# Performance work log

Measured on AMD Instinct MI355X. Metric: run time of the kernel, lower is better.

## Reference

```python
import jax, jax.numpy as jnp
import numpy as np

N = 50000      # amino-acid nodes
DIN = 64       # input feature dim
DH = 64        # hidden dim (= GAT out_feats per head)
H = 4          # attention heads
E_RES, E_SEQ, E_KNN = 400000, 100000, 400000
EPS = 1e-5


def setup_inputs() -> dict:
    key = jax.random.key(0)
    ks = iter(jax.random.split(key, 32))
    def nrm(shape, scale=0.1):
        return jax.random.normal(next(ks), shape, dtype=jnp.float32) * scale
    def edges(E):
        s = jax.random.randint(next(ks), (E,), 0, N, dtype=jnp.int32)
        d = jax.random.randint(next(ks), (E,), 0, N, dtype=jnp.int32)
        return s, d
    x = nrm((N, DIN), 1.0)
    src_res, dst_res = edges(E_RES)
    src_seq, dst_seq = edges(E_SEQ)
    src_knn, dst_knn = edges(E_KNN)
    inp = dict(x=x, src_res=src_res, dst_res=dst_res, src_seq=src_seq,
               dst_seq=dst_seq, src_knn=src_knn, dst_knn=dst_knn)
    # layer 0 (in=DIN), layer 1 (in=DH): per-relation stacked GAT params
    inp.update(W0=nrm((3, DIN, H * DH)), al0=nrm((3, H, DH)), ar0=nrm((3, H, DH)),
               b0=nrm((3, H * DH)), rW0=nrm((3, DIN, H * DH)))
    inp.update(W1=nrm((3, DH, H * DH)), al1=nrm((3, H, DH)), ar1=nrm((3, H, DH)),
               b1=nrm((3, H * DH)), rW1=nrm((3, DH, H * DH)))
    inp.update(fcW0=nrm((DH, DH)), fcb0=nrm((DH,)), fcW1=nrm((DH, DH)), fcb1=nrm((DH,)))
    inp.update(g0=jnp.ones((DIN,), jnp.float32), be0=jnp.zeros((DIN,), jnp.float32),
               g1=jnp.ones((DH,), jnp.float32), be1=jnp.zeros((DH,), jnp.float32))
    return inp


def _bn(x, g, b):
    mu = jnp.mean(x, axis=0)
    var = jnp.mean((x - mu) ** 2, axis=0)
    return (x - mu) * jax.lax.rsqrt(var + EPS) * g + b


def _gat(h, src, dst, W, al, ar, bias, rW):
    # DGL GATConv (feat_drop off in eval, residual=True via res_fc Linear, bias)
    n = h.shape[0]
    fs = (h @ W).reshape(n, H, DH)                    # [N,H,D]
    el = jnp.sum(fs * al, axis=-1)                    # [N,H]
    er = jnp.sum(fs * ar, axis=-1)
    e = jax.nn.leaky_relu(el[src] + er[dst], 0.2)     # [E,H]
    m = jax.ops.segment_max(e, dst, num_segments=n)
    a = jnp.exp(e - m[dst])
    s = jax.ops.segment_sum(a, dst, num_segments=n)
    alpha = a / s[dst]                                # edge-softmax per dst/head
    rst = jax.ops.segment_sum(alpha[:, :, None] * fs[src], dst, num_segments=n)
    return rst + (h @ rW).reshape(n, H, DH) + bias.reshape(1, H, DH)


def _layer(x, edges, W, al, ar, b, rW, fcW, fcb, g, be):
    x = _bn(x, g, be)
    h = jnp.zeros((x.shape[0], H, DH), x.dtype)
    for r, (s_, d_) in enumerate(edges):              # 3 relation types, summed
        h = h + _gat(x, s_, d_, W[r], al[r], ar[r], b[r], rW[r])
    x = jnp.mean(h, axis=1)                           # mean over heads
    return jax.nn.relu(x @ fcW + fcb)


def reference(x, src_res, dst_res, src_seq, dst_seq, src_knn, dst_knn,
              W0, al0, ar0, b0, rW0, W1, al1, ar1, b1, rW1,
              fcW0, fcb0, fcW1, fcb1, g0, be0, g1, be1):
    edges = [(src_res, dst_res), (src_seq, dst_seq), (src_knn, dst_knn)]
    x = _layer(x, edges, W0, al0, ar0, b0, rW0, fcW0, fcb0, g0, be0)
    x = _layer(x, edges, W1, al1, ar1, b1, rW1, fcW1, fcb1, g1, be1)
    return x
```

## Files before the change

### kernel.cpp

```cpp
#include <hip/hip_runtime.h>
#include <math.h>

#define NN    50000
#define DD    64
#define HH    4
#define E_RES 400000
#define E_SEQ 100000
#define E_KNN 400000
#define ETOT  (E_RES+E_SEQ+E_KNN)
#define RPS   (NN + 4)
#define NBLK  ((NN+255)/256)
#define KTOT  864
#define CTPS  (ETOT + 32)
#define NBUK  98
#define TBUK  (3*NBUK)
#define EPB   4096
#define PABLK ((ETOT+EPB-1)/EPB)
#define FBLK  (NN/16)
#define LZS   810

typedef __attribute__((ext_vector_type(8))) short short8;
typedef __attribute__((ext_vector_type(4))) float floatx4;

__device__ inline unsigned short f2bf(float f){
  union{float f; unsigned u;} v; v.f=f;
  unsigned r = v.u + 0x7FFF + ((v.u>>16)&1);
  return (unsigned short)(r>>16);
}
__device__ inline float bf2f(unsigned short u){
  union{unsigned u; float f;} v; v.u=(unsigned)u<<16; return v.f;
}

__global__ void __launch_bounds__(256)
k_bucketcnt(const int* __restrict__ d0, const int* __restrict__ d1,
            const int* __restrict__ d2, int* __restrict__ bcnt){
  __shared__ int cnt[TBUK];
  int t = threadIdx.x;
  for(int i=t;i<TBUK;i+=256) cnt[i]=0;
  __syncthreads();
  int ebase = blockIdx.x*EPB;
  #pragma unroll
  for(int j=0;j<16;j++){
    int i = ebase + j*256 + t;
    int d, r;
    if(i < E_RES){ d=d0[i]; r=0; }
    else if(i < E_RES+E_SEQ){ d=d1[i-E_RES]; r=1; }
    else if(i < ETOT){ d=d2[i-E_RES-E_SEQ]; r=2; }
    else continue;
    atomicAdd(&cnt[r*NBUK + (d>>9)], 1);
  }
  __syncthreads();
  for(int i=t;i<TBUK;i+=256){ int c=cnt[i]; if(c) atomicAdd(&bcnt[i], c); }
}

__global__ void k_bucketscan(const int* __restrict__ bcnt,
                             int* __restrict__ bbase, int* __restrict__ bcur){
  __shared__ int sh[TBUK];
  int t = threadIdx.x;
  if(t < 64){
    int carry = 0;
    for(int c=0;c<5;c++){
      int idx = c*64 + t;
      int v = (idx < TBUK) ? bcnt[idx] : 0;
      int inc = v;
      for(int off=1; off<64; off<<=1){ int n=__shfl_up(inc, off, 64); if(t>=off) inc+=n; }
      if(idx < TBUK) sh[idx] = carry + inc - v;
      carry += __shfl(inc, 63, 64);
    }
  }
  __syncthreads();
  if(t < TBUK){ bbase[t] = sh[t]; bcur[t] = sh[t]; }
  if(t == 0) bbase[TBUK] = ETOT;
}

__global__ void __launch_bounds__(256)
k_partA(const int* __restrict__ s0, const int* __restrict__ d0,
        const int* __restrict__ s1, const int* __restrict__ d1,
        const int* __restrict__ s2, const int* __restrict__ d2,
        int* __restrict__ bcur, unsigned* __restrict__ pairs){
  __shared__ int cnt[TBUK];
  __shared__ int gb[TBUK];
  int t = threadIdx.x;
  for(int i=t;i<TBUK;i+=256) cnt[i]=0;
  __syncthreads();
  int ebase = blockIdx.x*EPB;
  unsigned meta[16], pk[16];
  #pragma unroll
  for(int j=0;j<16;j++){
    int i = ebase + j*256 + t;
    int s, d, r;
    if(i < E_RES){ s=s0[i]; d=d0[i]; r=0; }
    else if(i < E_RES+E_SEQ){ int k=i-E_RES; s=s1[k]; d=d1[k]; r=1; }
    else if(i < ETOT){ int k=i-E_RES-E_SEQ; s=s2[k]; d=d2[k]; r=2; }
    else { meta[j]=0xFFFFFFFFu; continue; }
    int bk = r*NBUK + (d>>9);
    int rk = atomicAdd(&cnt[bk], 1);
    meta[j] = ((unsigned)bk<<16) | (unsigned)rk;
    pk[j]   = ((unsigned)(d&511)<<16) | (unsigned)s;
  }
  __syncthreads();
  for(int i=t;i<TBUK;i+=256){ int c=cnt[i]; gb[i] = c ? atomicAdd(&bcur[i], c) : 0; }
  __syncthreads();
  #pragma unroll
  for(int j=0;j<16;j++){
    unsigned mt = meta[j];
    if(mt != 0xFFFFFFFFu)
      pairs[gb[mt>>16] + (mt & 0xFFFFu)] = pk[j];
  }
}

__global__ void __launch_bounds__(256)
k_partB(const unsigned* __restrict__ pairs, const int* __restrict__ bbase,
        int* __restrict__ rowptr, int* __restrict__ csr){
  int bb = blockIdx.x, r = bb / NBUK, b = bb - r*NBUK;
  int dbase = b*512, dmax = min(512, NN - dbase);
  int off = (r==0)?0:(r==1)?E_RES:(E_RES+E_SEQ);
  __shared__ int hist[512];
  __shared__ int curs[513];
  int t = threadIdx.x;
  hist[t]=0; hist[256+t]=0;
  __syncthreads();
  int beg = bbase[bb], end = bbase[bb+1];
  for(int i=beg+t; i<end; i+=256) atomicAdd(&hist[pairs[i]>>16], 1);
  __syncthreads();
  if(t < 64){
    int carry = 0;
    for(int c=0;c<8;c++){
      int v = hist[c*64+t];
      int inc = v;
      for(int o2=1; o2<64; o2<<=1){ int n=__shfl_up(inc, o2, 64); if(t>=o2) inc+=n; }
      curs[c*64+t] = (beg - off) + carry + inc - v;
      carry += __shfl(inc, 63, 64);
    }
    if(t==0) curs[512] = end - off;
  }
  __syncthreads();
  int* rp = rowptr + r*RPS + dbase;
  for(int i=t; i<=dmax; i+=256) rp[i] = curs[i];
  __syncthreads();
  for(int i=beg+t; i<end; i+=256){
    unsigned p = pairs[i];
    int pos = atomicAdd(&curs[p>>16], 1);
    csr[off + pos] = (int)(p & 0xFFFFu);
  }
}

__global__ void k_bnstats(const float* __restrict__ x, float* __restrict__ stats,
                          unsigned short* __restrict__ Abf){
  __shared__ float sh[512];
  int t = threadIdx.x, col = t & 63, rg = t >> 6;
  float s=0.f, q=0.f;
  for(int row = blockIdx.x*4 + rg; row < NN; row += gridDim.x*4){
    float v = x[(size_t)row*64 + col]; s += v; q += v*v;
    Abf[(size_t)row*64 + col] = f2bf(v);
  }
  sh[t]=s; sh[256+t]=q; __syncthreads();
  if(rg==0){
    s = sh[col]+sh[64+col]+sh[128+col]+sh[192+col];
    q = sh[256+col]+sh[320+col]+sh[384+col]+sh[448+col];
    atomicAdd(&stats[col], s); atomicAdd(&stats[64+col], q);
  }
}

__global__ void __launch_bounds__(256)
k_prep3(const float* __restrict__ stats, const float* __restrict__ g,
        const float* __restrict__ be, const float* __restrict__ W,
        const float* __restrict__ al, const float* __restrict__ ar,
        const float* __restrict__ b, const float* __restrict__ rW,
        const float* __restrict__ fcW, const float* __restrict__ fcb,
        float* __restrict__ wbufF){
  __shared__ float scale[64], shift[64];
  int t = threadIdx.x;
  if(t<64){
    float mu  = stats[t]*(1.0f/NN);
    float var = stats[64+t]*(1.0f/NN) - mu*mu;
    float sc  = g[t]*rsqrtf(var + 1e-5f);
    scale[t]=sc; shift[t]=be[t]-mu*sc;
  }
  __syncthreads();
  char* wb = (char*)wbufF;
  unsigned short* Wf = (unsigned short*)wbufF;
  float* biasF = (float*)(wb + 110592);
  int bid = blockIdx.x;
  if(bid < 52){
    __shared__ float fcWs[4096];
    for(int i=t;i<4096;i+=256) fcWs[i]=fcW[i];
    __syncthreads();
    int j = bid*16 + (t>>4);
    int cg = (t&15)*4;
    float Wrow[64];
    if(j < 64){
      for(int d=0; d<64; d++){
        float w=0.f;
        for(int r=0;r<3;r++)
          #pragma unroll
          for(int h=0;h<4;h++)
            w += rW[((size_t)(r*64+j))*256 + h*64 + d];
        Wrow[d] = scale[j]*0.25f*w;
      }
    } else {
      int jj = j-64;
      int r = jj>>8, dc = jj&255, h = dc&3, c = dc>>2;
      const float* Wp = W + ((size_t)(r*64+c))*256 + h*64;
      float sc = 0.25f*scale[c];
      #pragma unroll
      for(int d=0; d<64; d++) Wrow[d] = sc*Wp[d];
    }
    #pragma unroll
    for(int cc=0; cc<4; cc++){
      int col = cg+cc;
      float acc=0.f;
      #pragma unroll
      for(int d=0; d<64; d++) acc += Wrow[d]*fcWs[d*64+col];
      Wf[(size_t)col*KTOT + j] = f2bf(acc);
    }
  } else if(bid < 58){
    int wv = (bid-52)*4 + (t>>6);
    int r = wv >> 3, cc = wv & 7, h = cc & 3, k = t & 63;
    const float* av = ((cc>=4)?ar:al) + (r*HH+h)*64;
    const float* Wk = W + ((size_t)(r*64+k))*256 + h*64;
    float w=0.f;
    for(int d2=0; d2<64; d2++) w += Wk[d2]*av[d2];
    float* WelR = (float*)(wb + 110848 + r*2080);
    WelR[cc*64 + k] = scale[k]*w;
    float bp = shift[k]*w;
    for(int off=32; off; off>>=1) bp += __shfl_down(bp, off, 64);
    if(k==0) (WelR + 512)[cc] = bp;
  } else {
    __shared__ float S[3][64];
    __shared__ float BH[64];
    if(t<192){
      int r=t>>6, d=t&63;
      float s=0.f;
      #pragma unroll
      for(int h=0;h<4;h++){
        const float* Wp = W + (size_t)(r*64)*256 + h*64 + d;
        for(int k=0;k<64;k++) s += shift[k]*Wp[(size_t)k*256];
      }
      S[r][d]=0.25f*s;
    } else {
      int d = t-192;
      float s=0.f;
      for(int k=0;k<64;k++){
        float w=0.f;
        for(int r=0;r<3;r++)
          #pragma unroll
          for(int h=0;h<4;h++)
            w += rW[((size_t)(r*64+k))*256 + h*64 + d];
        s += shift[k]*0.25f*w;
      }
      float bb=0.f;
      for(int r=0;r<3;r++)
        #pragma unroll
        for(int h=0;h<4;h++) bb += b[r*256 + h*64 + d];
      BH[d] = s + 0.25f*bb;
    }
    __syncthreads();
    if(t<192){
      int r=t>>6, col=t&63;
      float acc=0.f;
      for(int d=0;d<64;d++) acc += S[r][d]*fcW[d*64+col];
      Wf[(size_t)col*KTOT + 832 + r] = f2bf(acc);
    } else {
      int col=t-192;
      float acc=0.f;
      for(int d=0;d<64;d++) acc += BH[d]*fcW[d*64+col];
      biasF[col] = acc + fcb[col];
    }
    if(t<64){
      for(int j=835;j<KTOT;j++) Wf[(size_t)t*KTOT + j] = 0;
    }
  }
}

__global__ void __launch_bounds__(256)
k_el3(const float* __restrict__ A, const float* __restrict__ wbufF,
      float* __restrict__ EL){
  int r = blockIdx.x / NBLK;
  const char* wb = (const char*)wbufF;
  const float* Wel = (const float*)(wb + 110848 + r*2080);
  const float* biasE = Wel + 512;
  float* ELr = EL + (size_t)r*NN*8;
  __shared__ float sw[512];
  __shared__ float sb[8];
  int t = threadIdx.x;
  sw[t]=Wel[t]; sw[256+t]=Wel[256+t];
  if(t<8) sb[t]=biasE[t];
  __syncthreads();
  int n = (blockIdx.x % NBLK)*256 + t;
  if(n>=NN) return;
  float acc[8];
  #pragma unroll
  for(int c=0;c<8;c++) acc[c]=sb[c];
  const float4* Ar = (const float4*)(A + (size_t)n*64);
  #pragma unroll
  for(int kq=0;kq<16;kq++){
    float4 a = Ar[kq];
    #pragma unroll
    for(int c=0;c<8;c++){
      const float* w = sw + c*64 + kq*4;
      acc[c] += a.x*w[0] + a.y*w[1] + a.z*w[2] + a.w*w[3];
    }
  }
  ((float4*)ELr)[n*2]   = make_float4(acc[0],acc[1],acc[2],acc[3]);
  ((float4*)ELr)[n*2+1] = make_float4(acc[4],acc[5],acc[6],acc[7]);
}

__global__ void __launch_bounds__(256)
k_edgecoef3(const float* __restrict__ EL, const int* __restrict__ rowptr,
            const int* __restrict__ csr, float4* __restrict__ etmp,
            unsigned short* __restrict__ coefT){
  int r = blockIdx.x / NBLK;
  const float* ELr = EL + (size_t)r*NN*8;
  const int* rp = rowptr + r*RPS;
  int off = (r==0)?0:(r==1)?E_RES:(E_RES+E_SEQ);
  const int* cs = csr + off;
  float4* et = etmp + off;
  unsigned short* t0 = coefT + off;
  unsigned short* t1 = coefT + (size_t)CTPS + off;
  unsigned short* t2 = coefT + (size_t)2*CTPS + off;
  unsigned short* t3 = coefT + (size_t)3*CTPS + off;
  int n = (blockIdx.x % NBLK)*256 + threadIdx.x;
  if(n>=NN) return;
  int beg = rp[n], end = rp[n+1];
  if(end<=beg) return;
  const float4 er = ((const float4*)ELr)[n*2+1];
  float m0=-1e30f,m1=-1e30f,m2=-1e30f,m3=-1e30f;
  float s0=0.f,s1=0.f,s2=0.f,s3=0.f;
  for(int i=beg;i<end;i++){
    int src = cs[i];
    float4 el = ((const float4*)ELr)[src*2];
    float e0=el.x+er.x, e1=el.y+er.y, e2=el.z+er.z, e3=el.w+er.w;
    e0 = e0>0.f? e0 : 0.2f*e0;
    e1 = e1>0.f? e1 : 0.2f*e1;
    e2 = e2>0.f? e2 : 0.2f*e2;
    e3 = e3>0.f? e3 : 0.2f*e3;
    et[i] = make_float4(e0,e1,e2,e3);
    float n0=fmaxf(m0,e0); s0=s0*__expf(m0-n0)+__expf(e0-n0); m0=n0;
    float n1=fmaxf(m1,e1); s1=s1*__expf(m1-n1)+__expf(e1-n1); m1=n1;
    float n2=fmaxf(m2,e2); s2=s2*__expf(m2-n2)+__expf(e2-n2); m2=n2;
    float n3=fmaxf(m3,e3); s3=s3*__expf(m3-n3)+__expf(e3-n3); m3=n3;
  }
  float r0=1.f/s0, r1=1.f/s1, r2=1.f/s2, r3=1.f/s3;
  for(int i=beg;i<end;i++){
    float4 e = et[i];
    t0[i] = f2bf(__expf(e.x-m0)*r0);
    t1[i] = f2bf(__expf(e.y-m1)*r1);
    t2[i] = f2bf(__expf(e.z-m2)*r2);
    t3[i] = f2bf(__expf(e.w-m3)*r3);
  }
}

__global__ void __launch_bounds__(256)
k_fused(const unsigned short* __restrict__ Abf, const int* __restrict__ rowptr,
        const int* __restrict__ csr, const unsigned short* __restrict__ coefT,
        const float* __restrict__ wbufF, float* __restrict__ out,
        unsigned short* __restrict__ Abf2, float* __restrict__ stats, int dostats){
  __shared__ unsigned short Zl[16*LZS];
  const unsigned short* Wf = (const unsigned short*)wbufF;
  const float* biasF = (const float*)((const char*)wbufF + 110592);
  int t = threadIdx.x, wv = t>>6, lane = t&63, m = lane&15, kq = lane>>4;
  int nb = blockIdx.x*16;
  int n4 = nb + wv*4;
  int nn = m>>2, h = m&3;
  for(int i=t; i<512; i+=256){ int nd=i>>5, j=i&31; if(j<29) Zl[nd*LZS+771+j]=0; }
  for(int r=0;r<3;r++){
    const int* rp = rowptr + r*RPS;
    int off = (r==0)?0:(r==1)?E_RES:(E_RES+E_SEQ);
    const int* cs = csr + off;
    const unsigned short* cT = coefT + (size_t)h*CTPS + off;
    int rpn  = rp[n4+nn];
    int rpn1 = rp[n4+nn+1];
    unsigned dg = (unsigned)(rpn1 - rpn);
    int beg = __shfl(rpn, 0, 64);
    int end = __shfl(rpn1, 15, 64);
    floatx4 acc0={0.f,0.f,0.f,0.f};
    floatx4 acc1={0.f,0.f,0.f,0.f};
    floatx4 acc2={0.f,0.f,0.f,0.f};
    floatx4 acc3={0.f,0.f,0.f,0.f};
    for(int eb = (beg & ~31); eb < end; eb += 32){
      int p0 = eb + kq*8;
      union { uint4 q; short8 v; } af;
      af.q = *(const uint4*)(cT + p0);
      int qd = p0 - rpn;
      unsigned w0 = (((unsigned)(qd+0)<dg)?0x0000FFFFu:0u) | (((unsigned)(qd+1)<dg)?0xFFFF0000u:0u);
      unsigned w1 = (((unsigned)(qd+2)<dg)?0x0000FFFFu:0u) | (((unsigned)(qd+3)<dg)?0xFFFF0000u:0u);
      unsigned w2 = (((unsigned)(qd+4)<dg)?0x0000FFFFu:0u) | (((unsigned)(qd+5)<dg)?0xFFFF0000u:0u);
      unsigned w3 = (((unsigned)(qd+6)<dg)?0x0000FFFFu:0u) | (((unsigned)(qd+7)<dg)?0xFFFF0000u:0u);
      af.q.x &= w0; af.q.y &= w1; af.q.z &= w2; af.q.w &= w3;
      const int* csp = cs + p0;
      int s0=csp[0],s1=csp[1],s2=csp[2],s3=csp[3],s4=csp[4],s5=csp[5],s6=csp[6],s7=csp[7];
      const unsigned short* q0 = Abf + ((size_t)s0<<6) + m;
      const unsigned short* q1 = Abf + ((size_t)s1<<6) + m;
      const unsigned short* q2 = Abf + ((size_t)s2<<6) + m;
      const unsigned short* q3 = Abf + ((size_t)s3<<6) + m;
      const unsigned short* q4 = Abf + ((size_t)s4<<6) + m;
      const unsigned short* q5 = Abf + ((size_t)s5<<6) + m;
      const unsigned short* q6 = Abf + ((size_t)s6<<6) + m;
      const unsigned short* q7 = Abf + ((size_t)s7<<6) + m;
      union { unsigned u[4]; short8 v; } b0,b1,b2,b3;
      b0.u[0]=(unsigned)q0[0] |((unsigned)q1[0]<<16);
      b0.u[1]=(unsigned)q2[0] |((unsigned)q3[0]<<16);
      b0.u[2]=(unsigned)q4[0] |((unsigned)q5[0]<<16);
      b0.u[3]=(unsigned)q6[0] |((unsigned)q7[0]<<16);
      b1.u[0]=(unsigned)q0[16]|((unsigned)q1[16]<<16);
      b1.u[1]=(unsigned)q2[16]|((unsigned)q3[16]<<16);
      b1.u[2]=(unsigned)q4[16]|((unsigned)q5[16]<<16);
      b1.u[3]=(unsigned)q6[16]|((unsigned)q7[16]<<16);
      b2.u[0]=(unsigned)q0[32]|((unsigned)q1[32]<<16);
      b2.u[1]=(unsigned)q2[32]|((unsigned)q3[32]<<16);
      b2.u[2]=(unsigned)q4[32]|((unsigned)q5[32]<<16);
      b2.u[3]=(unsigned)q6[32]|((unsigned)q7[32]<<16);
      b3.u[0]=(unsigned)q0[48]|((unsigned)q1[48]<<16);
      b3.u[1]=(unsigned)q2[48]|((unsigned)q3[48]<<16);
      b3.u[2]=(unsigned)q4[48]|((unsigned)q5[48]<<16);
      b3.u[3]=(unsigned)q6[48]|((unsigned)q7[48]<<16);
      acc0 = __builtin_amdgcn_mfma_f32_16x16x32_bf16(af.v, b0.v, acc0, 0,0,0);
      acc1 = __builtin_amdgcn_mfma_f32_16x16x32_bf16(af.v, b1.v, acc1, 0,0,0);
      acc2 = __builtin_amdgcn_mfma_f32_16x16x32_bf16(af.v, b2.v, acc2, 0,0,0);
      acc3 = __builtin_amdgcn_mfma_f32_16x16x32_bf16(af.v, b3.v, acc3, 0,0,0);
    }
    unsigned short* zrow = Zl + (wv*4+kq)*LZS + r*256 + m*4;
    ushort4 o;
    o.x=f2bf(acc0[0]); o.y=f2bf(acc0[1]); o.z=f2bf(acc0[2]); o.w=f2bf(acc0[3]);
    *(ushort4*)(zrow)       = o;
    o.x=f2bf(acc1[0]); o.y=f2bf(acc1[1]); o.z=f2bf(acc1[2]); o.w=f2bf(acc1[3]);
    *(ushort4*)(zrow + 64)  = o;
    o.x=f2bf(acc2[0]); o.y=f2bf(acc2[1]); o.z=f2bf(acc2[2]); o.w=f2bf(acc2[3]);
    *(ushort4*)(zrow + 128) = o;
    o.x=f2bf(acc3[0]); o.y=f2bf(acc3[1]); o.z=f2bf(acc3[2]); o.w=f2bf(acc3[3]);
    *(ushort4*)(zrow + 192) = o;
    int degk = __shfl((int)dg, kq<<2, 64);
    if(m==0)
      Zl[(wv*4+kq)*LZS + 768 + r] = degk>0 ? (unsigned short)0x3F80 : (unsigned short)0;
  }
  __syncthreads();
  floatx4 acc = {0.f,0.f,0.f,0.f};
  const unsigned short* Arow = Abf + (size_t)(nb+m)*64;
  const unsigned short* Zrow = Zl + m*LZS;
  #pragma unroll
  for(int kb=0; kb<27; kb++){
    short8 a;
    if(kb<2) a = *(const short8*)(Arow + kb*32 + kq*8);
    else     a = *(const short8*)(Zrow + (kb-2)*32 + kq*8);
    short8 b = *(const short8*)(Wf + (size_t)(wv*16+m)*KTOT + kb*32 + kq*8);
    acc = __builtin_amdgcn_mfma_f32_16x16x32_bf16(a, b, acc, 0,0,0);
  }
  int col = wv*16 + m;
  float bb = biasF[col];
  float sv=0.f, qv=0.f;
  #pragma unroll
  for(int ri=0; ri<4; ri++){
    int ro = nb + kq*4 + ri;
    float v = fmaxf(acc[ri] + bb, 0.f);
    out[(size_t)ro*64 + col] = v;
    if(dostats){
      Abf2[(size_t)ro*64 + col] = f2bf(v);
      sv += v; qv += v*v;
    }
  }
  if(dostats){
    sv += __shfl_xor(sv, 16, 64); qv += __shfl_xor(qv, 16, 64);
    sv += __shfl_xor(sv, 32, 64); qv += __shfl_xor(qv, 32, 64);
    if(kq==0){ atomicAdd(&stats[col], sv); atomicAdd(&stats[64+col], qv); }
  }
}

extern "C" void kernel_launch(void* const* d_in, const int* in_sizes, int n_in,
                              void* d_out, int out_size, void* d_ws, size_t ws_size,
                              hipStream_t stream){
  const float* x      =(const float*)d_in[0];
  const int* src_res  =(const int*)d_in[1];
  const int* dst_res  =(const int*)d_in[2];
  const int* src_seq  =(const int*)d_in[3];
  const int* dst_seq  =(const int*)d_in[4];
  const int* src_knn  =(const int*)d_in[5];
  const int* dst_knn  =(const int*)d_in[6];
  const float* W0 =(const float*)d_in[7];
  const float* al0=(const float*)d_in[8];
  const float* ar0=(const float*)d_in[9];
  const float* b0 =(const float*)d_in[10];
  const float* rW0=(const float*)d_in[11];
  const float* W1 =(const float*)d_in[12];
  const float* al1=(const float*)d_in[13];
  const float* ar1=(const float*)d_in[14];
  const float* b1 =(const float*)d_in[15];
  const float* rW1=(const float*)d_in[16];
  const float* fcW0=(const float*)d_in[17];
  const float* fcb0=(const float*)d_in[18];
  const float* fcW1=(const float*)d_in[19];
  const float* fcb1=(const float*)d_in[20];
  const float* g0 =(const float*)d_in[21];
  const float* be0=(const float*)d_in[22];
  const float* g1 =(const float*)d_in[23];
  const float* be1=(const float*)d_in[24];

  char* ws=(char*)d_ws;
  int*   bcnt   =(int*)  (ws+0);
  int*   bbase  =(int*)  (ws+4096);
  float* stats0 =(float*)(ws+600000);
  float* stats1 =(float*)(ws+600512);
  int*   rowptr =(int*)  (ws+601024);
  int*   bcur   =(int*)  (ws+1201088);
  int*   csr    =(int*)  (ws+1801088);
  float* wbuf   =(float*)(ws+5401088);
  unsigned short* Abf  =(unsigned short*)(ws+5526528);
  float4* etmp  =(float4*)(ws+11926528UL);
  unsigned* pairs =(unsigned*)(ws+27000000UL);
  float* xbuf   =(float*)(ws+91926528UL);
  float* EL     =(float*)(ws+104726528UL);
  unsigned short* coefT=(unsigned short*)(ws+109526528UL);
  unsigned short* Abf2 =(unsigned short*)(ws+123926528UL);

  hipMemsetAsync(ws, 0, 601024, stream);

  k_bucketcnt<<<PABLK,256,0,stream>>>(dst_res,dst_seq,dst_knn,bcnt);
  k_bucketscan<<<1,512,0,stream>>>(bcnt,bbase,bcur);
  k_partA<<<PABLK,256,0,stream>>>(src_res,dst_res,src_seq,dst_seq,
                                  src_knn,dst_knn,bcur,pairs);
  k_partB<<<TBUK,256,0,stream>>>(pairs,bbase,rowptr,csr);

  k_bnstats<<<256,256,0,stream>>>(x,stats0,Abf);
  k_prep3<<<59,256,0,stream>>>(stats0,g0,be0,W0,al0,ar0,b0,rW0,fcW0,fcb0,wbuf);
  k_el3<<<3*NBLK,256,0,stream>>>(x,wbuf,EL);
  k_edgecoef3<<<3*NBLK,256,0,stream>>>(EL,rowptr,csr,etmp,coefT);
  k_fused<<<FBLK,256,0,stream>>>(Abf,rowptr,csr,coefT,wbuf,xbuf,Abf2,stats1,1);
  k_prep3<<<59,256,0,stream>>>(stats1,g1,be1,W1,al1,ar1,b1,rW1,fcW1,fcb1,wbuf);
  k_el3<<<3*NBLK,256,0,stream>>>(xbuf,wbuf,EL);
  k_edgecoef3<<<3*NBLK,256,0,stream>>>(EL,rowptr,csr,etmp,coefT);
  k_fused<<<FBLK,256,0,stream>>>(Abf2,rowptr,csr,coefT,wbuf,(float*)d_out,Abf2,stats0,0);
}
```

Baseline: 441.7 us.

## Split edge-softmax across 8 lanes per node and drop etmp buffer

The edge-softmax coefficient kernel now gives each (relation,node) pair to 8 lanes instead of one thread. Each lane covers a strided subset of edges with an online max/sum, and the lanes merge through shuffles. The first 32 edge scores stay in registers, and any beyond that are recomputed by gathering again, so the float4 etmp scratch write and reread is gone. This targets serial per-thread loops over degree and the extra memory traffic, at the cost of idle lanes on low-degree nodes and some recomputed gathers.

```diff
diff --git a/kernel.cpp b/kernel.cpp
--- a/kernel.cpp
+++ b/kernel.cpp
@@ -17,6 +17,7 @@
 #define EPB   4096
 #define PABLK ((ETOT+EPB-1)/EPB)
 #define FBLK  (NN/16)
+#define ECB2  ((3*NN + 31)/32)
 #define LZS   810
 
 typedef __attribute__((ext_vector_type(8))) short short8;
@@ -306,48 +307,78 @@
   ((float4*)ELr)[n*2+1] = make_float4(acc[4],acc[5],acc[6],acc[7]);
 }
 
+#define EC_GATHER(ii, E0,E1,E2,E3) { \
+    int src_ = cs[ii]; \
+    float4 el_ = ((const float4*)ELr)[src_*2]; \
+    E0=el_.x+er.x; E1=el_.y+er.y; E2=el_.z+er.z; E3=el_.w+er.w; \
+    E0 = E0>0.f? E0 : 0.2f*E0; \
+    E1 = E1>0.f? E1 : 0.2f*E1; \
+    E2 = E2>0.f? E2 : 0.2f*E2; \
+    E3 = E3>0.f? E3 : 0.2f*E3; }
+#define EC_ACC(E0,E1,E2,E3) { \
+    float n0_=fmaxf(m0,E0); s0=s0*__expf(m0-n0_)+__expf(E0-n0_); m0=n0_; \
+    float n1_=fmaxf(m1,E1); s1=s1*__expf(m1-n1_)+__expf(E1-n1_); m1=n1_; \
+    float n2_=fmaxf(m2,E2); s2=s2*__expf(m2-n2_)+__expf(E2-n2_); m2=n2_; \
+    float n3_=fmaxf(m3,E3); s3=s3*__expf(m3-n3_)+__expf(E3-n3_); m3=n3_; }
+#define EC_COMB(o) { \
+    float om_,os_,nm_; \
+    om_=__shfl_xor(m0,o,64); os_=__shfl_xor(s0,o,64); \
+    nm_=fmaxf(m0,om_); s0=s0*__expf(m0-nm_)+os_*__expf(om_-nm_); m0=nm_; \
+    om_=__shfl_xor(m1,o,64); os_=__shfl_xor(s1,o,64); \
+    nm_=fmaxf(m1,om_); s1=s1*__expf(m1-nm_)+os_*__expf(om_-nm_); m1=nm_; \
+    om_=__shfl_xor(m2,o,64); os_=__shfl_xor(s2,o,64); \
+    nm_=fmaxf(m2,om_); s2=s2*__expf(m2-nm_)+os_*__expf(om_-nm_); m2=nm_; \
+    om_=__shfl_xor(m3,o,64); os_=__shfl_xor(s3,o,64); \
+    nm_=fmaxf(m3,om_); s3=s3*__expf(m3-nm_)+os_*__expf(om_-nm_); m3=nm_; }
+#define EC_STORE(ii, E0,E1,E2,E3) { \
+    t0[ii]=f2bf(__expf(E0-m0)*r0); t1[ii]=f2bf(__expf(E1-m1)*r1); \
+    t2[ii]=f2bf(__expf(E2-m2)*r2); t3[ii]=f2bf(__expf(E3-m3)*r3); }
+
 __global__ void __launch_bounds__(256)
 k_edgecoef3(const float* __restrict__ EL, const int* __restrict__ rowptr,
-            const int* __restrict__ csr, float4* __restrict__ etmp,
-            unsigned short* __restrict__ coefT){
-  int r = blockIdx.x / NBLK;
+            const int* __restrict__ csr, unsigned short* __restrict__ coefT){
+  int item = blockIdx.x*32 + (threadIdx.x>>3);
+  int sl = threadIdx.x & 7;
+  if(item >= 3*NN) return;
+  int r = item / NN, n = item - r*NN;
   const float* ELr = EL + (size_t)r*NN*8;
   const int* rp = rowptr + r*RPS;
   int off = (r==0)?0:(r==1)?E_RES:(E_RES+E_SEQ);
   const int* cs = csr + off;
-  float4* et = etmp + off;
   unsigned short* t0 = coefT + off;
   unsigned short* t1 = coefT + (size_t)CTPS + off;
   unsigned short* t2 = coefT + (size_t)2*CTPS + off;
   unsigned short* t3 = coefT + (size_t)3*CTPS + off;
-  int n = (blockIdx.x % NBLK)*256 + threadIdx.x;
-  if(n>=NN) return;
   int beg = rp[n], end = rp[n+1];
-  if(end<=beg) return;
+  if(end <= beg) return;
   const float4 er = ((const float4*)ELr)[n*2+1];
   float m0=-1e30f,m1=-1e30f,m2=-1e30f,m3=-1e30f;
   float s0=0.f,s1=0.f,s2=0.f,s3=0.f;
-  for(int i=beg;i<end;i++){
-    int src = cs[i];
-    float4 el = ((const float4*)ELr)[src*2];
-    float e0=el.x+er.x, e1=el.y+er.y, e2=el.z+er.z, e3=el.w+er.w;
-    e0 = e0>0.f? e0 : 0.2f*e0;
-    e1 = e1>0.f? e1 : 0.2f*e1;
-    e2 = e2>0.f? e2 : 0.2f*e2;
-    e3 = e3>0.f? e3 : 0.2f*e3;
-    et[i] = make_float4(e0,e1,e2,e3);
-    float n0=fmaxf(m0,e0); s0=s0*__expf(m0-n0)+__expf(e0-n0); m0=n0;
-    float n1=fmaxf(m1,e1); s1=s1*__expf(m1-n1)+__expf(e1-n1); m1=n1;
-    float n2=fmaxf(m2,e2); s2=s2*__expf(m2-n2)+__expf(e2-n2); m2=n2;
-    float n3=fmaxf(m3,e3); s3=s3*__expf(m3-n3)+__expf(e3-n3); m3=n3;
-  }
+  int i0 = beg + sl, i1 = i0 + 8, i2 = i0 + 16, i3 = i0 + 24;
+  bool h0 = i0 < end, h1 = i1 < end, h2 = i2 < end, h3 = i3 < end;
+  float a0=0.f,a1=0.f,a2=0.f,a3=0.f;
+  float b0=0.f,b1=0.f,b2=0.f,b3=0.f;
+  float c0=0.f,c1=0.f,c2=0.f,c3=0.f;
+  float d0=0.f,d1=0.f,d2=0.f,d3=0.f;
+  if(h0){ EC_GATHER(i0, a0,a1,a2,a3); EC_ACC(a0,a1,a2,a3); }
+  if(h1){ EC_GATHER(i1, b0,b1,b2,b3); EC_ACC(b0,b1,b2,b3); }
+  if(h2){ EC_GATHER(i2, c0,c1,c2,c3); EC_ACC(c0,c1,c2,c3); }
+  if(h3){ EC_GATHER(i3, d0,d1,d2,d3); EC_ACC(d0,d1,d2,d3); }
+  for(int i = i0 + 32; i < end; i += 8){
+    float e0,e1,e2,e3;
+    EC_GATHER(i, e0,e1,e2,e3);
+    EC_ACC(e0,e1,e2,e3);
+  }
+  EC_COMB(1) EC_COMB(2) EC_COMB(4)
   float r0=1.f/s0, r1=1.f/s1, r2=1.f/s2, r3=1.f/s3;
-  for(int i=beg;i<end;i++){
-    float4 e = et[i];
-    t0[i] = f2bf(__expf(e.x-m0)*r0);
-    t1[i] = f2bf(__expf(e.y-m1)*r1);
-    t2[i] = f2bf(__expf(e.z-m2)*r2);
-    t3[i] = f2bf(__expf(e.w-m3)*r3);
+  if(h0) EC_STORE(i0, a0,a1,a2,a3);
+  if(h1) EC_STORE(i1, b0,b1,b2,b3);
+  if(h2) EC_STORE(i2, c0,c1,c2,c3);
+  if(h3) EC_STORE(i3, d0,d1,d2,d3);
+  for(int i = i0 + 32; i < end; i += 8){
+    float e0,e1,e2,e3;
+    EC_GATHER(i, e0,e1,e2,e3);
+    EC_STORE(i, e0,e1,e2,e3);
   }
 }
 
@@ -505,7 +536,6 @@
   int*   csr    =(int*)  (ws+1801088);
   float* wbuf   =(float*)(ws+5401088);
   unsigned short* Abf  =(unsigned short*)(ws+5526528);
-  float4* etmp  =(float4*)(ws+11926528UL);
   unsigned* pairs =(unsigned*)(ws+27000000UL);
   float* xbuf   =(float*)(ws+91926528UL);
   float* EL     =(float*)(ws+104726528UL);
@@ -523,10 +553,10 @@
   k_bnstats<<<256,256,0,stream>>>(x,stats0,Abf);
   k_prep3<<<59,256,0,stream>>>(stats0,g0,be0,W0,al0,ar0,b0,rW0,fcW0,fcb0,wbuf);
   k_el3<<<3*NBLK,256,0,stream>>>(x,wbuf,EL);
-  k_edgecoef3<<<3*NBLK,256,0,stream>>>(EL,rowptr,csr,etmp,coefT);
+  k_edgecoef3<<<ECB2,256,0,stream>>>(EL,rowptr,csr,coefT);
   k_fused<<<FBLK,256,0,stream>>>(Abf,rowptr,csr,coefT,wbuf,xbuf,Abf2,stats1,1);
   k_prep3<<<59,256,0,stream>>>(stats1,g1,be1,W1,al1,ar1,b1,rW1,fcW1,fcb1,wbuf);
   k_el3<<<3*NBLK,256,0,stream>>>(xbuf,wbuf,EL);
-  k_edgecoef3<<<3*NBLK,256,0,stream>>>(EL,rowptr,csr,etmp,coefT);
+  k_edgecoef3<<<ECB2,256,0,stream>>>(EL,rowptr,csr,coefT);
   k_fused<<<FBLK,256,0,stream>>>(Abf2,rowptr,csr,coefT,wbuf,(float*)d_out,Abf2,stats0,0);
 }
```

Result: faster. 409.0 us (-7.4%).
